# Kernel optimization log

Measured on AMD Instinct MI355X. Metric: run time of the kernel, lower is better.

## Reference

```python
import jax, jax.numpy as jnp
import numpy as np

DIM = 256
HEADS = 8
B, T, D, H, W = 2, 8, 16, 16, 16


def _mha(x, wqkv, bqkv, wo, bo):
    # x: [M, S, F]; standard self-attention (q=k=v=x), LoRA rank 0.
    M, S, F = x.shape
    hd = F // HEADS
    qkv = jnp.einsum('msf,kfg->kmsg', x, wqkv) + bqkv[:, None, None, :]  # [3,M,S,F]
    q, k, v = qkv
    q = q.reshape(M, S, HEADS, hd).transpose(0, 2, 1, 3)  # [M,Hh,S,hd]
    k = k.reshape(M, S, HEADS, hd).transpose(0, 2, 1, 3)
    v = v.reshape(M, S, HEADS, hd).transpose(0, 2, 1, 3)
    scores = jnp.einsum('mhsd,mhtd->mhst', q, k) / jnp.sqrt(jnp.asarray(hd, x.dtype))
    attn = jax.nn.softmax(scores, axis=-1)
    out = jnp.einsum('mhst,mhtd->mhsd', attn, v)
    out = out.transpose(0, 2, 1, 3).reshape(M, S, F)
    return out @ wo + bo


def _make_params(key, name_suffix):
    k1, k2 = jax.random.split(key)
    s = 1.0 / np.sqrt(DIM)
    return {
        f'wqkv_{name_suffix}': jax.random.normal(k1, (3, DIM, DIM), jnp.float32) * s,
        f'bqkv_{name_suffix}': jnp.zeros((3, DIM), jnp.float32),
        f'wo_{name_suffix}': jax.random.normal(k2, (DIM, DIM), jnp.float32) * s,
        f'bo_{name_suffix}': jnp.zeros((DIM,), jnp.float32),
    }


def setup_inputs() -> dict:
    key = jax.random.key(0)
    ks = jax.random.split(key, 5)
    inp = {'x': jax.random.normal(ks[0], (B, T, D * H * W, DIM), jnp.float32)}
    for k, ax in zip(ks[1:], ['t', 'd', 'h', 'w']):
        inp.update(_make_params(k, ax))
    inp['grid_d'] = D
    inp['grid_h'] = H
    inp['grid_w'] = W
    return inp


def reference(x, wqkv_t, bqkv_t, wo_t, bo_t,
              wqkv_d, bqkv_d, wo_d, bo_d,
              wqkv_h, bqkv_h, wo_h, bo_h,
              wqkv_w, bqkv_w, wo_w, bo_w,
              grid_d, grid_h, grid_w):
    b, t, n, f = x.shape
    d, h, w = grid_d, grid_h, grid_w
    x = x.reshape(b, t, d, h, w, f)
    if t > 1:
        xt = x.transpose(0, 2, 3, 4, 1, 5).reshape(b * d * h * w, t, f)
        xt = _mha(xt, wqkv_t, bqkv_t, wo_t, bo_t)
        xt = xt.reshape(b, d, h, w, t, f).transpose(0, 4, 1, 2, 3, 5)
        x = x + xt
    xd = x.transpose(0, 1, 3, 4, 2, 5).reshape(b * t * h * w, d, f)
    xd = _mha(xd, wqkv_d, bqkv_d, wo_d, bo_d)
    xd = xd.reshape(b, t, h, w, d, f).transpose(0, 1, 4, 2, 3, 5)
    xh = x.transpose(0, 1, 2, 4, 3, 5).reshape(b * t * d * w, h, f)
    xh = _mha(xh, wqkv_h, bqkv_h, wo_h, bo_h)
    xh = xh.reshape(b, t, d, w, h, f).transpose(0, 1, 2, 4, 3, 5)
    xw = x.reshape(b * t * d * h, w, f)
    xw = _mha(xw, wqkv_w, bqkv_w, wo_w, bo_w)
    xw = xw.reshape(b, t, d, h, w, f)
    x_comb = x + xd + xh + xw
    return x_comb.reshape(b, t, d * h * w, f)
```

## Files before the change

kernel.cpp:

```cpp
#include <hip/hip_runtime.h>

typedef __attribute__((ext_vector_type(4))) float f32x4;
typedef __attribute__((ext_vector_type(8))) short s16x8;

__device__ __forceinline__ ushort f2bf(float f) {
  union { float f; uint u; } v; v.f = f;
  uint r = v.u + 0x7fffu + ((v.u >> 16) & 1u);
  return (ushort)(r >> 16);
}

__device__ __forceinline__ void glds16(const void* g, void* l) {
  __builtin_amdgcn_global_load_lds(
      (const __attribute__((address_space(1))) uint*)g,
      (__attribute__((address_space(3))) uint*)l, 16, 0, 0);
}

__device__ __forceinline__ int asidx(int row, int col) {
  return row*256 + ((((col>>3) ^ (row & 7)))<<3) + (col&7);
}
__device__ __forceinline__ int scridx(int row, int col) {
  return row*32 + ((((col>>3) ^ ((row>>2)&3)))<<3) + (col&7);
}
__device__ __forceinline__ int epidx(int row, int f) {
  return row*256 + (f ^ ((row & 7) << 2));
}

struct WSrc { const float* p[8]; };

__global__ __launch_bounds__(256) void prep_weights(WSrc s, ushort* wq, ushort* wo) {
  int mm = blockIdx.x >> 6;
  int t  = blockIdx.x & 63;
  int a = mm >> 2, sub = mm & 3;
  const float* src = (sub < 3) ? (s.p[a*2] + sub*65536) : s.p[a*2+1];
  ushort*      dst = (sub < 3) ? (wq + (a*3 + sub)*65536) : (wo + a*65536);
  int gt = (t >> 3) * 32, ft = (t & 7) * 32;
  __shared__ float tile[32][33];
  int lx = threadIdx.x & 31, ly = threadIdx.x >> 5;
#pragma unroll
  for (int i = 0; i < 4; i++)
    tile[ly + i*8][lx] = src[(ft + ly + i*8)*256 + gt + lx];
  __syncthreads();
#pragma unroll
  for (int i = 0; i < 4; i++) {
    int n = gt + ly + i*8, col = ft + lx;
    dst[asidx(n, col)] = f2bf(tile[lx][ly + i*8]);
  }
}

template<int AXIS>
__device__ __forceinline__ int token_index(int blk, int row) {
  if (AXIS == 0) {
    int seq = blk*8 + (row >> 3);
    int t = row & 7;
    int b = seq >> 12, n = seq & 4095;
    return (b*8 + t)*4096 + n;
  } else {
    int sid = blk*4 + (row >> 4);
    int bt = sid >> 8, lo = sid & 255, r = row & 15;
    if (AXIS == 1) { int hh = lo >> 4, ww = lo & 15; return bt*4096 + r*256 + hh*16 + ww; }
    if (AXIS == 2) { int dd = lo >> 4, ww = lo & 15; return bt*4096 + dd*256 + r*16 + ww; }
    { int dd = lo >> 4, hh = lo & 15; return bt*4096 + dd*256 + hh*16 + r; }
  }
}

#define PUB_BARRIER() do { \
    __builtin_amdgcn_sched_barrier(0); \
    asm volatile("s_waitcnt lgkmcnt(0)" ::: "memory"); \
    __builtin_amdgcn_sched_barrier(0); \
    __builtin_amdgcn_s_barrier(); \
    __builtin_amdgcn_sched_barrier(0); } while (0)

template<int AXIS>
__global__ __launch_bounds__(256, 2) void axial_pass(
    const float* __restrict__ x0, const ushort* __restrict__ xb,
    const ushort* __restrict__ wqkvT, const float* __restrict__ bqkv,
    const ushort* __restrict__ woT, const float* __restrict__ bo,
    float* __restrict__ out, ushort* __restrict__ x1b) {

  __shared__ ushort smem[40960];
  ushort* Wb0 = smem;
  ushort* Wb1 = smem + 8192;
  ushort* AsT = smem + 16384;
  ushort* Scr = smem + 32768;

  const int tid = threadIdx.x, blk = blockIdx.x;
  const int wv = tid >> 6, lane = tid & 63, llo = lane & 15, lhi = lane >> 4;
  const int rg = wv >> 1, ch = wv & 1;
  const f32x4 fzero = {0.f, 0.f, 0.f, 0.f};
  const s16x8 szero = {0,0,0,0,0,0,0,0};

  auto issue_stage = [&](int s) {
    const ushort* src = (s < 24) ? (wqkvT + (s % 3)*65536 + (s / 3)*8192)
                                 : (woT + (s - 24)*8192);
    const ushort* g = src + wv*2048 + lane*8;
    ushort* l = ((s & 1) ? Wb1 : Wb0) + wv*2048;
#pragma unroll
    for (int i = 0; i < 4; i++) glds16(g + i*512, l + i*512);
  };

#define STAGE_SYNC(sn) do { \
    __builtin_amdgcn_sched_barrier(0); \
    asm volatile("s_waitcnt vmcnt(0) lgkmcnt(0)" ::: "memory"); \
    __builtin_amdgcn_sched_barrier(0); \
    __builtin_amdgcn_s_barrier(); \
    __builtin_amdgcn_sched_barrier(0); \
    if ((sn) < 32) issue_stage(sn); \
  } while (0)

  issue_stage(0);

  {
    int row = tid >> 2, q = tid & 3;
    int tok = token_index<AXIS>(blk, row);
    if (AXIS == 0) {
      const float4* s4 = (const float4*)(x0 + (size_t)tok*256 + q*64);
#pragma unroll
      for (int c2 = 0; c2 < 8; c2++) {
        float4 v0 = s4[c2*2], v1 = s4[c2*2 + 1];
        s16x8 o;
        o[0] = (short)f2bf(v0.x); o[1] = (short)f2bf(v0.y);
        o[2] = (short)f2bf(v0.z); o[3] = (short)f2bf(v0.w);
        o[4] = (short)f2bf(v1.x); o[5] = (short)f2bf(v1.y);
        o[6] = (short)f2bf(v1.z); o[7] = (short)f2bf(v1.w);
        *(s16x8*)(AsT + asidx(row, (q*8 + c2)*8)) = o;
      }
    } else {
      const s16x8* s8 = (const s16x8*)(xb + (size_t)tok*256 + q*64);
#pragma unroll
      for (int c2 = 0; c2 < 8; c2++)
        *(s16x8*)(AsT + asidx(row, (q*8 + c2)*8)) = s8[c2];
    }
  }
  {
    ushort* Vtw = Scr + wv*2048 + 1024;
    *(s16x8*)(Vtw + scridx(lane >> 1, 16 + (lane & 1)*8)) = szero;
  }
  __syncthreads();

  s16x8 af[2][8];
#pragma unroll
  for (int g = 0; g < 2; g++)
#pragma unroll
    for (int ks = 0; ks < 8; ks++)
      af[g][ks] = *(const s16x8*)(AsT + asidx(rg*32 + g*16 + llo, (ks*4 + lhi)*8));

  auto proj2 = [&](int sb, f32x4& c0, f32x4& c1) {
    const ushort* buf = sb ? Wb1 : Wb0;
    __builtin_amdgcn_s_setprio(1);
#pragma unroll
    for (int ks = 0; ks < 8; ks++) {
      s16x8 bv = *(const s16x8*)(buf + asidx(ch*16 + llo, (ks*4 + lhi)*8));
      c0 = __builtin_amdgcn_mfma_f32_16x16x32_bf16(af[0][ks], bv, c0, 0, 0, 0);
      c1 = __builtin_amdgcn_mfma_f32_16x16x32_bf16(af[1][ks], bv, c1, 0, 0, 0);
    }
    __builtin_amdgcn_s_setprio(0);
  };

#pragma unroll 1
  for (int h = 0; h < 8; h++) {
    STAGE_SYNC(3*h + 1);
    {
      f32x4 c0 = fzero, c1 = fzero;
      proj2((3*h) & 1, c0, c1);
      float bi = bqkv[h*32 + ch*16 + llo];
      ushort* q0 = Scr + (rg*2 + 0)*2048;
      ushort* q1 = Scr + (rg*2 + 1)*2048;
#pragma unroll
      for (int r = 0; r < 4; r++) {
        q0[scridx(lhi*4 + r, ch*16 + llo)] = f2bf(c0[r] + bi);
        q1[scridx(lhi*4 + r, ch*16 + llo)] = f2bf(c1[r] + bi);
      }
    }
    STAGE_SYNC(3*h + 2);
    {
      f32x4 c0 = fzero, c1 = fzero;
      proj2((3*h + 1) & 1, c0, c1);
      float bi = bqkv[256 + h*32 + ch*16 + llo];
      ushort* k0 = Scr + (rg*2 + 0)*2048 + 512;
      ushort* k1 = Scr + (rg*2 + 1)*2048 + 512;
#pragma unroll
      for (int r = 0; r < 4; r++) {
        k0[scridx(lhi*4 + r, ch*16 + llo)] = f2bf(c0[r] + bi);
        k1[scridx(lhi*4 + r, ch*16 + llo)] = f2bf(c1[r] + bi);
      }
    }
    STAGE_SYNC(3*h + 3);
    {
      f32x4 c0 = fzero, c1 = fzero;
      proj2((3*h + 2) & 1, c0, c1);
      float bi = bqkv[512 + h*32 + ch*16 + llo];
      ushort* v0 = Scr + (rg*2 + 0)*2048 + 1024;
      ushort* v1 = Scr + (rg*2 + 1)*2048 + 1024;
#pragma unroll
      for (int r = 0; r < 4; r++) {
        v0[scridx(ch*16 + llo, lhi*4 + r)] = f2bf(c0[r] + bi);
        v1[scridx(ch*16 + llo, lhi*4 + r)] = f2bf(c1[r] + bi);
      }
    }
    PUB_BARRIER();

    {
      ushort* S = Scr + wv*2048;
      s16x8 aq = *(const s16x8*)(S + scridx(llo, lhi*8));
      s16x8 bk = *(const s16x8*)(S + 512 + scridx(llo, lhi*8));
      f32x4 sc = __builtin_amdgcn_mfma_f32_16x16x32_bf16(aq, bk, fzero, 0, 0, 0);
#pragma unroll
      for (int r = 0; r < 4; r++) {
        float sv = sc[r] * 0.17677669529663689f;
        if (AXIS == 0) {
          int srow = lhi*4 + r;
          if ((srow >> 3) != (llo >> 3)) sv = -1e30f;
        }
        float mx = sv;
        mx = fmaxf(mx, __shfl_xor(mx, 1));
        mx = fmaxf(mx, __shfl_xor(mx, 2));
        mx = fmaxf(mx, __shfl_xor(mx, 4));
        mx = fmaxf(mx, __shfl_xor(mx, 8));
        float e = __expf(sv - mx);
        float sm = e;
        sm += __shfl_xor(sm, 1);
        sm += __shfl_xor(sm, 2);
        sm += __shfl_xor(sm, 4);
        sm += __shfl_xor(sm, 8);
        (S + 512)[scridx(lhi*4 + r, llo)] = f2bf(e * __builtin_amdgcn_rcpf(sm));
      }
      s16x8 ap  = *(const s16x8*)(S + 512 + scridx(llo, lhi*8));
      s16x8 bv0 = *(const s16x8*)(S + 1024 + scridx(llo, lhi*8));
      s16x8 bv1 = *(const s16x8*)(S + 1024 + scridx(16 + llo, lhi*8));
      f32x4 o0 = __builtin_amdgcn_mfma_f32_16x16x32_bf16(ap, bv0, fzero, 0, 0, 0);
      f32x4 o1 = __builtin_amdgcn_mfma_f32_16x16x32_bf16(ap, bv1, fzero, 0, 0, 0);
#pragma unroll
      for (int r = 0; r < 4; r++) {
        AsT[asidx(wv*16 + lhi*4 + r, h*32 + llo)]      = f2bf(o0[r]);
        AsT[asidx(wv*16 + lhi*4 + r, h*32 + 16 + llo)] = f2bf(o1[r]);
      }
    }
  }

  PUB_BARRIER();

#pragma unroll
  for (int g = 0; g < 2; g++)
#pragma unroll
    for (int ks = 0; ks < 8; ks++)
      af[g][ks] = *(const s16x8*)(AsT + asidx(rg*32 + g*16 + llo, (ks*4 + lhi)*8));

  f32x4 acc[16];
#pragma unroll
  for (int i = 0; i < 16; i++) acc[i] = fzero;
#pragma unroll
  for (int st = 0; st < 8; st++) {
    STAGE_SYNC(25 + st);
    const ushort* buf = (st & 1) ? Wb1 : Wb0;
    __builtin_amdgcn_s_setprio(1);
#pragma unroll
    for (int ks = 0; ks < 8; ks++) {
      s16x8 bv = *(const s16x8*)(buf + asidx(ch*16 + llo, (ks*4 + lhi)*8));
      acc[st*2]   = __builtin_amdgcn_mfma_f32_16x16x32_bf16(af[0][ks], bv, acc[st*2],   0, 0, 0);
      acc[st*2+1] = __builtin_amdgcn_mfma_f32_16x16x32_bf16(af[1][ks], bv, acc[st*2+1], 0, 0, 0);
    }
    __builtin_amdgcn_s_setprio(0);
  }

  float* Fep = (float*)smem;
  PUB_BARRIER();
#pragma unroll
  for (int st = 0; st < 8; st++) {
#pragma unroll
    for (int g = 0; g < 2; g++) {
#pragma unroll
      for (int r = 0; r < 4; r++) {
        int row = rg*32 + g*16 + lhi*4 + r;
        Fep[epidx(row, st*32 + ch*16 + llo)] = acc[st*2 + g][r];
      }
    }
  }
  PUB_BARRIER();
  {
    int rbase = tid >> 3, g = tid & 7;
#pragma unroll 1
    for (int step = 0; step < 2; step++) {
      int row = rbase + step*32;
      int tok = token_index<AXIS>(blk, row);
      size_t base = (size_t)tok*256;
#pragma unroll
      for (int i = 0; i < 8; i++) {
        int f = i*32 + g*4;
        float4 v = *(float4*)&Fep[epidx(row, f)];
        float4 b = *(const float4*)&bo[f];
        v.x += b.x; v.y += b.y; v.z += b.z; v.w += b.w;
        if (AXIS == 0) {
          float4 x = *(const float4*)&x0[base + f];
          v.x += x.x; v.y += x.y; v.z += x.z; v.w += x.w;
          *(float4*)&out[base + f] = v;
          ushort4 p; p.x = f2bf(v.x); p.y = f2bf(v.y);
          p.z = f2bf(v.z); p.w = f2bf(v.w);
          *(ushort4*)&x1b[base + f] = p;
        } else {
          float4 o = *(float4*)&out[base + f];
          o.x += v.x; o.y += v.y; o.z += v.z; o.w += v.w;
          *(float4*)&out[base + f] = o;
        }
      }
    }
  }
#undef STAGE_SYNC
}

extern "C" void kernel_launch(void* const* d_in, const int* in_sizes, int n_in,
                              void* d_out, int out_size, void* d_ws, size_t ws_size,
                              hipStream_t stream) {
  const float* x = (const float*)d_in[0];
  ushort* wq  = (ushort*)d_ws;
  ushort* wo  = wq + 4*3*65536;
  ushort* x1b = wo + 4*65536;
  float* out = (float*)d_out;

  WSrc wsrc;
  wsrc.p[0] = (const float*)d_in[1];  wsrc.p[1] = (const float*)d_in[3];
  wsrc.p[2] = (const float*)d_in[5];  wsrc.p[3] = (const float*)d_in[7];
  wsrc.p[4] = (const float*)d_in[9];  wsrc.p[5] = (const float*)d_in[11];
  wsrc.p[6] = (const float*)d_in[13]; wsrc.p[7] = (const float*)d_in[15];
  prep_weights<<<dim3(1024), dim3(256), 0, stream>>>(wsrc, wq, wo);

  const float* bq_t = (const float*)d_in[2];  const float* bo_t = (const float*)d_in[4];
  const float* bq_d = (const float*)d_in[6];  const float* bo_d = (const float*)d_in[8];
  const float* bq_h = (const float*)d_in[10]; const float* bo_h = (const float*)d_in[12];
  const float* bq_w = (const float*)d_in[14]; const float* bo_w = (const float*)d_in[16];

  axial_pass<0><<<dim3(1024), dim3(256), 0, stream>>>(x, nullptr, wq + 0*3*65536, bq_t, wo + 0*65536, bo_t, out, x1b);
  axial_pass<1><<<dim3(1024), dim3(256), 0, stream>>>(nullptr, x1b, wq + 1*3*65536, bq_d, wo + 1*65536, bo_d, out, nullptr);
  axial_pass<2><<<dim3(1024), dim3(256), 0, stream>>>(nullptr, x1b, wq + 2*3*65536, bq_h, wo + 2*65536, bo_h, out, nullptr);
  axial_pass<3><<<dim3(1024), dim3(256), 0, stream>>>(nullptr, x1b, wq + 3*3*65536, bq_w, wo + 3*65536, bo_w, out, nullptr);
}
```

Baseline: 351.0 us.

## Double block size to 512 threads and keep attention output in registers

Each block now handles 128 token rows with 8 waves, so every streamed weight stage in LDS is reused by twice as many rows and only half as many blocks are launched. The separate activation buffer in LDS is dropped: input rows are staged through the scratch area in two halves, and each wave keeps its attention output fragments in registers for the output projection instead of writing them back to shared memory. The epilogue goes through LDS in bf16 rather than fp32, with wider 8-element accesses. The trade-off is higher register pressure from the extra fragments and the fully unrolled head loop, plus extra rounding of the projection result before the bias and residual add.

Result: slower. 415.7 us (+18.4%).

```diff
diff --git a/kernel.cpp b/kernel.cpp
--- a/kernel.cpp
+++ b/kernel.cpp
@@ -8,6 +8,9 @@
   uint r = v.u + 0x7fffu + ((v.u >> 16) & 1u);
   return (ushort)(r >> 16);
 }
+__device__ __forceinline__ float bf2f(ushort u) {
+  union { uint i; float f; } v; v.i = ((uint)u) << 16; return v.f;
+}
 
 __device__ __forceinline__ void glds16(const void* g, void* l) {
   __builtin_amdgcn_global_load_lds(
@@ -20,9 +23,6 @@
 }
 __device__ __forceinline__ int scridx(int row, int col) {
   return row*32 + ((((col>>3) ^ ((row>>2)&3)))<<3) + (col&7);
-}
-__device__ __forceinline__ int epidx(int row, int f) {
-  return row*256 + (f ^ ((row & 7) << 2));
 }
 
 struct WSrc { const float* p[8]; };
@@ -50,12 +50,12 @@
 template<int AXIS>
 __device__ __forceinline__ int token_index(int blk, int row) {
   if (AXIS == 0) {
-    int seq = blk*8 + (row >> 3);
+    int seq = blk*16 + (row >> 3);
     int t = row & 7;
     int b = seq >> 12, n = seq & 4095;
     return (b*8 + t)*4096 + n;
   } else {
-    int sid = blk*4 + (row >> 4);
+    int sid = blk*8 + (row >> 4);
     int bt = sid >> 8, lo = sid & 255, r = row & 15;
     if (AXIS == 1) { int hh = lo >> 4, ww = lo & 15; return bt*4096 + r*256 + hh*16 + ww; }
     if (AXIS == 2) { int dd = lo >> 4, ww = lo & 15; return bt*4096 + dd*256 + r*16 + ww; }
@@ -71,17 +71,16 @@
     __builtin_amdgcn_sched_barrier(0); } while (0)
 
 template<int AXIS>
-__global__ __launch_bounds__(256, 2) void axial_pass(
+__global__ __launch_bounds__(512, 4) void axial_pass(
     const float* __restrict__ x0, const ushort* __restrict__ xb,
     const ushort* __restrict__ wqkvT, const float* __restrict__ bqkv,
     const ushort* __restrict__ woT, const float* __restrict__ bo,
     float* __restrict__ out, ushort* __restrict__ x1b) {
 
-  __shared__ ushort smem[40960];
+  __shared__ ushort smem[32768];
   ushort* Wb0 = smem;
   ushort* Wb1 = smem + 8192;
-  ushort* AsT = smem + 16384;
-  ushort* Scr = smem + 32768;
+  ushort* Scr = smem + 16384;
 
   const int tid = threadIdx.x, blk = blockIdx.x;
   const int wv = tid >> 6, lane = tid & 63, llo = lane & 15, lhi = lane >> 4;
@@ -92,10 +91,10 @@
   auto issue_stage = [&](int s) {
     const ushort* src = (s < 24) ? (wqkvT + (s % 3)*65536 + (s / 3)*8192)
                                  : (woT + (s - 24)*8192);
-    const ushort* g = src + wv*2048 + lane*8;
-    ushort* l = ((s & 1) ? Wb1 : Wb0) + wv*2048;
-#pragma unroll
-    for (int i = 0; i < 4; i++) glds16(g + i*512, l + i*512);
+    const ushort* g = src + wv*1024 + lane*8;
+    ushort* l = ((s & 1) ? Wb1 : Wb0) + wv*1024;
+    glds16(g, l);
+    glds16(g + 512, l + 512);
   };
 
 #define STAGE_SYNC(sn) do { \
@@ -109,40 +108,57 @@
 
   issue_stage(0);
 
-  {
-    int row = tid >> 2, q = tid & 3;
-    int tok = token_index<AXIS>(blk, row);
+  s16x8 af[2][8];
+  auto stage_half = [&](int half) {
+    int row = tid >> 3, j = tid & 7;
+    int tok = token_index<AXIS>(blk, half*64 + row);
     if (AXIS == 0) {
-      const float4* s4 = (const float4*)(x0 + (size_t)tok*256 + q*64);
-#pragma unroll
-      for (int c2 = 0; c2 < 8; c2++) {
-        float4 v0 = s4[c2*2], v1 = s4[c2*2 + 1];
+      const float4* s4 = (const float4*)(x0 + (size_t)tok*256);
+#pragma unroll
+      for (int i = 0; i < 4; i++) {
+        int c = j + 8*i;
+        float4 v0 = s4[c*2], v1 = s4[c*2 + 1];
         s16x8 o;
         o[0] = (short)f2bf(v0.x); o[1] = (short)f2bf(v0.y);
         o[2] = (short)f2bf(v0.z); o[3] = (short)f2bf(v0.w);
         o[4] = (short)f2bf(v1.x); o[5] = (short)f2bf(v1.y);
         o[6] = (short)f2bf(v1.z); o[7] = (short)f2bf(v1.w);
-        *(s16x8*)(AsT + asidx(row, (q*8 + c2)*8)) = o;
+        *(s16x8*)(Scr + asidx(row, c*8)) = o;
       }
     } else {
-      const s16x8* s8 = (const s16x8*)(xb + (size_t)tok*256 + q*64);
-#pragma unroll
-      for (int c2 = 0; c2 < 8; c2++)
-        *(s16x8*)(AsT + asidx(row, (q*8 + c2)*8)) = s8[c2];
-    }
-  }
+      const s16x8* s8 = (const s16x8*)(xb + (size_t)tok*256);
+#pragma unroll
+      for (int i = 0; i < 4; i++) {
+        int c = j + 8*i;
+        *(s16x8*)(Scr + asidx(row, c*8)) = s8[c];
+      }
+    }
+  };
+
+  stage_half(0);
+  __syncthreads();
+  if (wv < 4) {
+#pragma unroll
+    for (int g = 0; g < 2; g++)
+#pragma unroll
+      for (int ks = 0; ks < 8; ks++)
+        af[g][ks] = *(const s16x8*)(Scr + asidx(rg*32 + g*16 + llo, (ks*4 + lhi)*8));
+  }
+  __syncthreads();
+  stage_half(1);
+  __syncthreads();
+  if (wv >= 4) {
+#pragma unroll
+    for (int g = 0; g < 2; g++)
+#pragma unroll
+      for (int ks = 0; ks < 8; ks++)
+        af[g][ks] = *(const s16x8*)(Scr + asidx((rg - 2)*32 + g*16 + llo, (ks*4 + lhi)*8));
+  }
+  __syncthreads();
   {
     ushort* Vtw = Scr + wv*2048 + 1024;
     *(s16x8*)(Vtw + scridx(lane >> 1, 16 + (lane & 1)*8)) = szero;
   }
-  __syncthreads();
-
-  s16x8 af[2][8];
-#pragma unroll
-  for (int g = 0; g < 2; g++)
-#pragma unroll
-    for (int ks = 0; ks < 8; ks++)
-      af[g][ks] = *(const s16x8*)(AsT + asidx(rg*32 + g*16 + llo, (ks*4 + lhi)*8));
 
   auto proj2 = [&](int sb, f32x4& c0, f32x4& c1) {
     const ushort* buf = sb ? Wb1 : Wb0;
@@ -156,7 +172,9 @@
     __builtin_amdgcn_s_setprio(0);
   };
 
-#pragma unroll 1
+  s16x8 af_o[8];
+
+#pragma unroll
   for (int h = 0; h < 8; h++) {
     STAGE_SYNC(3*h + 1);
     {
@@ -231,19 +249,12 @@
       f32x4 o1 = __builtin_amdgcn_mfma_f32_16x16x32_bf16(ap, bv1, fzero, 0, 0, 0);
 #pragma unroll
       for (int r = 0; r < 4; r++) {
-        AsT[asidx(wv*16 + lhi*4 + r, h*32 + llo)]      = f2bf(o0[r]);
-        AsT[asidx(wv*16 + lhi*4 + r, h*32 + 16 + llo)] = f2bf(o1[r]);
-      }
-    }
-  }
-
-  PUB_BARRIER();
-
-#pragma unroll
-  for (int g = 0; g < 2; g++)
-#pragma unroll
-    for (int ks = 0; ks < 8; ks++)
-      af[g][ks] = *(const s16x8*)(AsT + asidx(rg*32 + g*16 + llo, (ks*4 + lhi)*8));
+        S[scridx(lhi*4 + r, llo)]      = f2bf(o0[r]);
+        S[scridx(lhi*4 + r, 16 + llo)] = f2bf(o1[r]);
+      }
+      af_o[h] = *(const s16x8*)(S + scridx(llo, lhi*8));
+    }
+  }
 
   f32x4 acc[16];
 #pragma unroll
@@ -255,52 +266,59 @@
     __builtin_amdgcn_s_setprio(1);
 #pragma unroll
     for (int ks = 0; ks < 8; ks++) {
-      s16x8 bv = *(const s16x8*)(buf + asidx(ch*16 + llo, (ks*4 + lhi)*8));
-      acc[st*2]   = __builtin_amdgcn_mfma_f32_16x16x32_bf16(af[0][ks], bv, acc[st*2],   0, 0, 0);
-      acc[st*2+1] = __builtin_amdgcn_mfma_f32_16x16x32_bf16(af[1][ks], bv, acc[st*2+1], 0, 0, 0);
+      s16x8 b0 = *(const s16x8*)(buf + asidx(llo,      (ks*4 + lhi)*8));
+      s16x8 b1 = *(const s16x8*)(buf + asidx(16 + llo, (ks*4 + lhi)*8));
+      acc[st*2]   = __builtin_amdgcn_mfma_f32_16x16x32_bf16(af_o[ks], b0, acc[st*2],   0, 0, 0);
+      acc[st*2+1] = __builtin_amdgcn_mfma_f32_16x16x32_bf16(af_o[ks], b1, acc[st*2+1], 0, 0, 0);
     }
     __builtin_amdgcn_s_setprio(0);
   }
 
-  float* Fep = (float*)smem;
+  ushort* Fep = smem;
   PUB_BARRIER();
 #pragma unroll
   for (int st = 0; st < 8; st++) {
 #pragma unroll
-    for (int g = 0; g < 2; g++) {
-#pragma unroll
-      for (int r = 0; r < 4; r++) {
-        int row = rg*32 + g*16 + lhi*4 + r;
-        Fep[epidx(row, st*32 + ch*16 + llo)] = acc[st*2 + g][r];
+    for (int j = 0; j < 2; j++) {
+#pragma unroll
+      for (int r = 0; r < 4; r++) {
+        int row = wv*16 + lhi*4 + r;
+        Fep[asidx(row, st*32 + j*16 + llo)] = f2bf(acc[st*2 + j][r]);
       }
     }
   }
   PUB_BARRIER();
   {
-    int rbase = tid >> 3, g = tid & 7;
-#pragma unroll 1
-    for (int step = 0; step < 2; step++) {
-      int row = rbase + step*32;
-      int tok = token_index<AXIS>(blk, row);
-      size_t base = (size_t)tok*256;
-#pragma unroll
-      for (int i = 0; i < 8; i++) {
-        int f = i*32 + g*4;
-        float4 v = *(float4*)&Fep[epidx(row, f)];
-        float4 b = *(const float4*)&bo[f];
-        v.x += b.x; v.y += b.y; v.z += b.z; v.w += b.w;
-        if (AXIS == 0) {
-          float4 x = *(const float4*)&x0[base + f];
-          v.x += x.x; v.y += x.y; v.z += x.z; v.w += x.w;
-          *(float4*)&out[base + f] = v;
-          ushort4 p; p.x = f2bf(v.x); p.y = f2bf(v.y);
-          p.z = f2bf(v.z); p.w = f2bf(v.w);
-          *(ushort4*)&x1b[base + f] = p;
-        } else {
-          float4 o = *(float4*)&out[base + f];
-          o.x += v.x; o.y += v.y; o.z += v.z; o.w += v.w;
-          *(float4*)&out[base + f] = o;
-        }
+    int row = tid >> 2, q = tid & 3;
+    int tok = token_index<AXIS>(blk, row);
+    size_t base = (size_t)tok*256;
+#pragma unroll
+    for (int i = 0; i < 8; i++) {
+      int col = q*64 + i*8;
+      s16x8 v8 = *(const s16x8*)(Fep + asidx(row, col));
+      float f[8];
+#pragma unroll
+      for (int j = 0; j < 8; j++) f[j] = bf2f((ushort)v8[j]) + bo[col + j];
+      if (AXIS == 0) {
+        float4 xa = *(const float4*)&x0[base + col];
+        float4 xb4 = *(const float4*)&x0[base + col + 4];
+        float4 va = {f[0]+xa.x, f[1]+xa.y, f[2]+xa.z, f[3]+xa.w};
+        float4 vb = {f[4]+xb4.x, f[5]+xb4.y, f[6]+xb4.z, f[7]+xb4.w};
+        *(float4*)&out[base + col]     = va;
+        *(float4*)&out[base + col + 4] = vb;
+        s16x8 p;
+        p[0] = (short)f2bf(va.x); p[1] = (short)f2bf(va.y);
+        p[2] = (short)f2bf(va.z); p[3] = (short)f2bf(va.w);
+        p[4] = (short)f2bf(vb.x); p[5] = (short)f2bf(vb.y);
+        p[6] = (short)f2bf(vb.z); p[7] = (short)f2bf(vb.w);
+        *(s16x8*)&x1b[base + col] = p;
+      } else {
+        float4 oa = *(float4*)&out[base + col];
+        float4 ob = *(float4*)&out[base + col + 4];
+        oa.x += f[0]; oa.y += f[1]; oa.z += f[2]; oa.w += f[3];
+        ob.x += f[4]; ob.y += f[5]; ob.z += f[6]; ob.w += f[7];
+        *(float4*)&out[base + col]     = oa;
+        *(float4*)&out[base + col + 4] = ob;
       }
     }
   }
@@ -328,8 +346,8 @@
   const float* bq_h = (const float*)d_in[10]; const float* bo_h = (const float*)d_in[12];
   const float* bq_w = (const float*)d_in[14]; const float* bo_w = (const float*)d_in[16];
 
-  axial_pass<0><<<dim3(1024), dim3(256), 0, stream>>>(x, nullptr, wq + 0*3*65536, bq_t, wo + 0*65536, bo_t, out, x1b);
-  axial_pass<1><<<dim3(1024), dim3(256), 0, stream>>>(nullptr, x1b, wq + 1*3*65536, bq_d, wo + 1*65536, bo_d, out, nullptr);
-  axial_pass<2><<<dim3(1024), dim3(256), 0, stream>>>(nullptr, x1b, wq + 2*3*65536, bq_h, wo + 2*65536, bo_h, out, nullptr);
-  axial_pass<3><<<dim3(1024), dim3(256), 0, stream>>>(nullptr, x1b, wq + 3*3*65536, bq_w, wo + 3*65536, bo_w, out, nullptr);
-}
+  axial_pass<0><<<dim3(512), dim3(512), 0, stream>>>(x, nullptr, wq + 0*3*65536, bq_t, wo + 0*65536, bo_t, out, x1b);
+  axial_pass<1><<<dim3(512), dim3(512), 0, stream>>>(nullptr, x1b, wq + 1*3*65536, bq_d, wo + 1*65536, bo_d, out, nullptr);
+  axial_pass<2><<<dim3(512), dim3(512), 0, stream>>>(nullptr, x1b, wq + 2*3*65536, bq_h, wo + 2*65536, bo_h, out, nullptr);
+  axial_pass<3><<<dim3(512), dim3(512), 0, stream>>>(nullptr, x1b, wq + 3*3*65536, bq_w, wo + 3*65536, bo_w, out, nullptr);
+}
```

## Fuse output projection into per-head loop and shrink LDS for higher occupancy

Applied to the files above, without the earlier changes.

The output projection now runs per head inside the attention loop. Each head's attention output (16 rows x 32 dims per wave) is multiplied against a head-sliced Wo tile that prep_weights reorders into a new layout, and the results accumulate in registers. This removes the full-width attention-output staging buffer in LDS, cutting shared memory from 80KB to 48KB so launch bounds can allow 3 blocks per CU. In exchange the epilogue now rounds the fp32 projection accumulators to bf16 in LDS before adding the bias and residual, which loses precision. The kernel also issues one extra stage sync per head.

Result: slower. 462.9 us (+31.9%).

```diff
diff --git a/kernel.cpp b/kernel.cpp
--- a/kernel.cpp
+++ b/kernel.cpp
@@ -8,6 +8,9 @@
   uint r = v.u + 0x7fffu + ((v.u >> 16) & 1u);
   return (ushort)(r >> 16);
 }
+__device__ __forceinline__ float bf2f(ushort u) {
+  union { uint i; float f; } v; v.i = ((uint)u) << 16; return v.f;
+}
 
 __device__ __forceinline__ void glds16(const void* g, void* l) {
   __builtin_amdgcn_global_load_lds(
@@ -20,9 +23,6 @@
 }
 __device__ __forceinline__ int scridx(int row, int col) {
   return row*32 + ((((col>>3) ^ ((row>>2)&3)))<<3) + (col&7);
-}
-__device__ __forceinline__ int epidx(int row, int f) {
-  return row*256 + (f ^ ((row & 7) << 2));
 }
 
 struct WSrc { const float* p[8]; };
@@ -42,8 +42,10 @@
   __syncthreads();
 #pragma unroll
   for (int i = 0; i < 4; i++) {
-    int n = gt + ly + i*8, col = ft + lx;
-    dst[asidx(n, col)] = f2bf(tile[lx][ly + i*8]);
+    int n = gt + ly + i*8, k = ft + lx;
+    float v = tile[lx][ly + i*8];
+    if (sub < 3) dst[asidx(n, k)] = f2bf(v);
+    else         dst[(k >> 5)*8192 + (n >> 4)*512 + scridx(n & 15, k & 31)] = f2bf(v);
   }
 }
 
@@ -71,17 +73,16 @@
     __builtin_amdgcn_sched_barrier(0); } while (0)
 
 template<int AXIS>
-__global__ __launch_bounds__(256, 2) void axial_pass(
+__global__ __launch_bounds__(256, 3) void axial_pass(
     const float* __restrict__ x0, const ushort* __restrict__ xb,
     const ushort* __restrict__ wqkvT, const float* __restrict__ bqkv,
-    const ushort* __restrict__ woT, const float* __restrict__ bo,
+    const ushort* __restrict__ woR, const float* __restrict__ bo,
     float* __restrict__ out, ushort* __restrict__ x1b) {
 
-  __shared__ ushort smem[40960];
+  __shared__ ushort smem[24576];
   ushort* Wb0 = smem;
   ushort* Wb1 = smem + 8192;
-  ushort* AsT = smem + 16384;
-  ushort* Scr = smem + 32768;
+  ushort* Scr = smem + 16384;
 
   const int tid = threadIdx.x, blk = blockIdx.x;
   const int wv = tid >> 6, lane = tid & 63, llo = lane & 15, lhi = lane >> 4;
@@ -90,8 +91,9 @@
   const s16x8 szero = {0,0,0,0,0,0,0,0};
 
   auto issue_stage = [&](int s) {
-    const ushort* src = (s < 24) ? (wqkvT + (s % 3)*65536 + (s / 3)*8192)
-                                 : (woT + (s - 24)*8192);
+    int h = s >> 2, m = s & 3;
+    const ushort* src = (m < 3) ? (wqkvT + m*65536 + h*8192)
+                                 : (woR + h*8192);
     const ushort* g = src + wv*2048 + lane*8;
     ushort* l = ((s & 1) ? Wb1 : Wb0) + wv*2048;
 #pragma unroll
@@ -106,8 +108,6 @@
     __builtin_amdgcn_sched_barrier(0); \
     if ((sn) < 32) issue_stage(sn); \
   } while (0)
-
-  issue_stage(0);
 
   {
     int row = tid >> 2, q = tid & 3;
@@ -122,13 +122,13 @@
         o[2] = (short)f2bf(v0.z); o[3] = (short)f2bf(v0.w);
         o[4] = (short)f2bf(v1.x); o[5] = (short)f2bf(v1.y);
         o[6] = (short)f2bf(v1.z); o[7] = (short)f2bf(v1.w);
-        *(s16x8*)(AsT + asidx(row, (q*8 + c2)*8)) = o;
+        *(s16x8*)(smem + asidx(row, (q*8 + c2)*8)) = o;
       }
     } else {
       const s16x8* s8 = (const s16x8*)(xb + (size_t)tok*256 + q*64);
 #pragma unroll
       for (int c2 = 0; c2 < 8; c2++)
-        *(s16x8*)(AsT + asidx(row, (q*8 + c2)*8)) = s8[c2];
+        *(s16x8*)(smem + asidx(row, (q*8 + c2)*8)) = s8[c2];
     }
   }
   {
@@ -142,7 +142,10 @@
   for (int g = 0; g < 2; g++)
 #pragma unroll
     for (int ks = 0; ks < 8; ks++)
-      af[g][ks] = *(const s16x8*)(AsT + asidx(rg*32 + g*16 + llo, (ks*4 + lhi)*8));
+      af[g][ks] = *(const s16x8*)(smem + asidx(rg*32 + g*16 + llo, (ks*4 + lhi)*8));
+  __syncthreads();
+
+  issue_stage(0);
 
   auto proj2 = [&](int sb, f32x4& c0, f32x4& c1) {
     const ushort* buf = sb ? Wb1 : Wb0;
@@ -156,12 +159,16 @@
     __builtin_amdgcn_s_setprio(0);
   };
 
+  f32x4 acc[16];
+#pragma unroll
+  for (int i = 0; i < 16; i++) acc[i] = fzero;
+
 #pragma unroll 1
   for (int h = 0; h < 8; h++) {
-    STAGE_SYNC(3*h + 1);
+    STAGE_SYNC(4*h + 1);
     {
       f32x4 c0 = fzero, c1 = fzero;
-      proj2((3*h) & 1, c0, c1);
+      proj2((4*h) & 1, c0, c1);
       float bi = bqkv[h*32 + ch*16 + llo];
       ushort* q0 = Scr + (rg*2 + 0)*2048;
       ushort* q1 = Scr + (rg*2 + 1)*2048;
@@ -171,10 +178,10 @@
         q1[scridx(lhi*4 + r, ch*16 + llo)] = f2bf(c1[r] + bi);
       }
     }
-    STAGE_SYNC(3*h + 2);
+    STAGE_SYNC(4*h + 2);
     {
       f32x4 c0 = fzero, c1 = fzero;
-      proj2((3*h + 1) & 1, c0, c1);
+      proj2((4*h + 1) & 1, c0, c1);
       float bi = bqkv[256 + h*32 + ch*16 + llo];
       ushort* k0 = Scr + (rg*2 + 0)*2048 + 512;
       ushort* k1 = Scr + (rg*2 + 1)*2048 + 512;
@@ -184,10 +191,11 @@
         k1[scridx(lhi*4 + r, ch*16 + llo)] = f2bf(c1[r] + bi);
       }
     }
-    STAGE_SYNC(3*h + 3);
+    STAGE_SYNC(4*h + 3);
+    s16x8 af_o;
     {
       f32x4 c0 = fzero, c1 = fzero;
-      proj2((3*h + 2) & 1, c0, c1);
+      proj2((4*h + 2) & 1, c0, c1);
       float bi = bqkv[512 + h*32 + ch*16 + llo];
       ushort* v0 = Scr + (rg*2 + 0)*2048 + 1024;
       ushort* v1 = Scr + (rg*2 + 1)*2048 + 1024;
@@ -196,10 +204,8 @@
         v0[scridx(ch*16 + llo, lhi*4 + r)] = f2bf(c0[r] + bi);
         v1[scridx(ch*16 + llo, lhi*4 + r)] = f2bf(c1[r] + bi);
       }
-    }
-    PUB_BARRIER();
-
-    {
+      PUB_BARRIER();
+
       ushort* S = Scr + wv*2048;
       s16x8 aq = *(const s16x8*)(S + scridx(llo, lhi*8));
       s16x8 bk = *(const s16x8*)(S + 512 + scridx(llo, lhi*8));
@@ -231,49 +237,32 @@
       f32x4 o1 = __builtin_amdgcn_mfma_f32_16x16x32_bf16(ap, bv1, fzero, 0, 0, 0);
 #pragma unroll
       for (int r = 0; r < 4; r++) {
-        AsT[asidx(wv*16 + lhi*4 + r, h*32 + llo)]      = f2bf(o0[r]);
-        AsT[asidx(wv*16 + lhi*4 + r, h*32 + 16 + llo)] = f2bf(o1[r]);
-      }
-    }
-  }
-
+        S[scridx(lhi*4 + r, llo)]      = f2bf(o0[r]);
+        S[scridx(lhi*4 + r, 16 + llo)] = f2bf(o1[r]);
+      }
+      af_o = *(const s16x8*)(S + scridx(llo, lhi*8));
+    }
+    STAGE_SYNC(4*h + 4);
+    {
+      const ushort* buf = ((4*h + 3) & 1) ? Wb1 : Wb0;
+      const int so = scridx(llo, lhi*8);
+      __builtin_amdgcn_s_setprio(1);
+#pragma unroll
+      for (int nb = 0; nb < 16; nb++) {
+        s16x8 bw = *(const s16x8*)(buf + nb*512 + so);
+        acc[nb] = __builtin_amdgcn_mfma_f32_16x16x32_bf16(af_o, bw, acc[nb], 0, 0, 0);
+      }
+      __builtin_amdgcn_s_setprio(0);
+    }
+  }
+
+  ushort* Fep = smem;
   PUB_BARRIER();
-
-#pragma unroll
-  for (int g = 0; g < 2; g++)
-#pragma unroll
-    for (int ks = 0; ks < 8; ks++)
-      af[g][ks] = *(const s16x8*)(AsT + asidx(rg*32 + g*16 + llo, (ks*4 + lhi)*8));
-
-  f32x4 acc[16];
-#pragma unroll
-  for (int i = 0; i < 16; i++) acc[i] = fzero;
-#pragma unroll
-  for (int st = 0; st < 8; st++) {
-    STAGE_SYNC(25 + st);
-    const ushort* buf = (st & 1) ? Wb1 : Wb0;
-    __builtin_amdgcn_s_setprio(1);
-#pragma unroll
-    for (int ks = 0; ks < 8; ks++) {
-      s16x8 bv = *(const s16x8*)(buf + asidx(ch*16 + llo, (ks*4 + lhi)*8));
-      acc[st*2]   = __builtin_amdgcn_mfma_f32_16x16x32_bf16(af[0][ks], bv, acc[st*2],   0, 0, 0);
-      acc[st*2+1] = __builtin_amdgcn_mfma_f32_16x16x32_bf16(af[1][ks], bv, acc[st*2+1], 0, 0, 0);
-    }
-    __builtin_amdgcn_s_setprio(0);
-  }
-
-  float* Fep = (float*)smem;
-  PUB_BARRIER();
-#pragma unroll
-  for (int st = 0; st < 8; st++) {
-#pragma unroll
-    for (int g = 0; g < 2; g++) {
-#pragma unroll
-      for (int r = 0; r < 4; r++) {
-        int row = rg*32 + g*16 + lhi*4 + r;
-        Fep[epidx(row, st*32 + ch*16 + llo)] = acc[st*2 + g][r];
-      }
-    }
+#pragma unroll
+  for (int nb = 0; nb < 16; nb++) {
+#pragma unroll
+    for (int r = 0; r < 4; r++)
+      Fep[asidx(wv*16 + lhi*4 + r, nb*16 + llo)] = f2bf(acc[nb][r]);
   }
   PUB_BARRIER();
   {
@@ -285,21 +274,22 @@
       size_t base = (size_t)tok*256;
 #pragma unroll
       for (int i = 0; i < 8; i++) {
-        int f = i*32 + g*4;
-        float4 v = *(float4*)&Fep[epidx(row, f)];
-        float4 b = *(const float4*)&bo[f];
-        v.x += b.x; v.y += b.y; v.z += b.z; v.w += b.w;
+        int col = i*32 + g*4;
+        const ushort* fp = Fep + asidx(row, col);
+        float4 b = *(const float4*)&bo[col];
+        float4 v = {bf2f(fp[0]) + b.x, bf2f(fp[1]) + b.y,
+                    bf2f(fp[2]) + b.z, bf2f(fp[3]) + b.w};
         if (AXIS == 0) {
-          float4 x = *(const float4*)&x0[base + f];
+          float4 x = *(const float4*)&x0[base + col];
           v.x += x.x; v.y += x.y; v.z += x.z; v.w += x.w;
-          *(float4*)&out[base + f] = v;
+          *(float4*)&out[base + col] = v;
           ushort4 p; p.x = f2bf(v.x); p.y = f2bf(v.y);
           p.z = f2bf(v.z); p.w = f2bf(v.w);
-          *(ushort4*)&x1b[base + f] = p;
+          *(ushort4*)&x1b[base + col] = p;
         } else {
-          float4 o = *(float4*)&out[base + f];
+          float4 o = *(float4*)&out[base + col];
           o.x += v.x; o.y += v.y; o.z += v.z; o.w += v.w;
-          *(float4*)&out[base + f] = o;
+          *(float4*)&out[base + col] = o;
         }
       }
     }
```

## Use per-wave private weight buffers with vmcnt pipelining to drop block barriers

Applied to the files above, without the earlier changes.

The QKV projection weight staging changes from a block-shared double buffer guarded by a full barrier per stage to per-wave private copies of each wave's column half. These are prefetched two stages ahead and waited on with a partial vmcnt, so most block-wide barriers in the projection loop disappear. Each wave's attention output is now kept in registers and written back to a shared A tile only once, after the head loop. The cost is twice the weight bytes loaded into LDS, since both row-group waves fetch the same slice, plus a full unroll of the head loop that raises register pressure.

Measured after the change: 392.4 us. 1.12x slower.

```diff
diff --git a/kernel.cpp b/kernel.cpp
--- a/kernel.cpp
+++ b/kernel.cpp
@@ -78,9 +78,6 @@
     float* __restrict__ out, ushort* __restrict__ x1b) {
 
   __shared__ ushort smem[40960];
-  ushort* Wb0 = smem;
-  ushort* Wb1 = smem + 8192;
-  ushort* AsT = smem + 16384;
   ushort* Scr = smem + 32768;
 
   const int tid = threadIdx.x, blk = blockIdx.x;
@@ -89,25 +86,24 @@
   const f32x4 fzero = {0.f, 0.f, 0.f, 0.f};
   const s16x8 szero = {0,0,0,0,0,0,0,0};
 
-  auto issue_stage = [&](int s) {
-    const ushort* src = (s < 24) ? (wqkvT + (s % 3)*65536 + (s / 3)*8192)
-                                 : (woT + (s - 24)*8192);
-    const ushort* g = src + wv*2048 + lane*8;
-    ushort* l = ((s & 1) ? Wb1 : Wb0) + wv*2048;
-#pragma unroll
-    for (int i = 0; i < 4; i++) glds16(g + i*512, l + i*512);
+  auto issue_priv = [&](int s) {
+    const ushort* g = wqkvT + (s % 3)*65536 + (s / 3)*8192 + ch*4096 + lane*8;
+    ushort* l = smem + (s & 1)*16384 + wv*4096 + lane*8;
+#pragma unroll
+    for (int i = 0; i < 8; i++) glds16(g + i*512, l + i*512);
   };
 
-#define STAGE_SYNC(sn) do { \
-    __builtin_amdgcn_sched_barrier(0); \
-    asm volatile("s_waitcnt vmcnt(0) lgkmcnt(0)" ::: "memory"); \
-    __builtin_amdgcn_sched_barrier(0); \
-    __builtin_amdgcn_s_barrier(); \
-    __builtin_amdgcn_sched_barrier(0); \
-    if ((sn) < 32) issue_stage(sn); \
+#define WAIT_STAGE(s) do { \
+    if ((s) <= 22) { asm volatile("s_waitcnt vmcnt(8)" ::: "memory"); } \
+    else           { asm volatile("s_waitcnt vmcnt(0)" ::: "memory"); } \
+    __builtin_amdgcn_sched_barrier(0); \
   } while (0)
-
-  issue_stage(0);
+#define ISSUE_NEXT(s) do { \
+    __builtin_amdgcn_sched_barrier(0); \
+    asm volatile("s_waitcnt lgkmcnt(0)" ::: "memory"); \
+    __builtin_amdgcn_sched_barrier(0); \
+    if ((s) + 2 <= 23) issue_priv((s) + 2); \
+  } while (0)
 
   {
     int row = tid >> 2, q = tid & 3;
@@ -122,13 +118,13 @@
         o[2] = (short)f2bf(v0.z); o[3] = (short)f2bf(v0.w);
         o[4] = (short)f2bf(v1.x); o[5] = (short)f2bf(v1.y);
         o[6] = (short)f2bf(v1.z); o[7] = (short)f2bf(v1.w);
-        *(s16x8*)(AsT + asidx(row, (q*8 + c2)*8)) = o;
+        *(s16x8*)(smem + asidx(row, (q*8 + c2)*8)) = o;
       }
     } else {
       const s16x8* s8 = (const s16x8*)(xb + (size_t)tok*256 + q*64);
 #pragma unroll
       for (int c2 = 0; c2 < 8; c2++)
-        *(s16x8*)(AsT + asidx(row, (q*8 + c2)*8)) = s8[c2];
+        *(s16x8*)(smem + asidx(row, (q*8 + c2)*8)) = s8[c2];
     }
   }
   {
@@ -142,26 +138,30 @@
   for (int g = 0; g < 2; g++)
 #pragma unroll
     for (int ks = 0; ks < 8; ks++)
-      af[g][ks] = *(const s16x8*)(AsT + asidx(rg*32 + g*16 + llo, (ks*4 + lhi)*8));
-
-  auto proj2 = [&](int sb, f32x4& c0, f32x4& c1) {
-    const ushort* buf = sb ? Wb1 : Wb0;
-    __builtin_amdgcn_s_setprio(1);
-#pragma unroll
-    for (int ks = 0; ks < 8; ks++) {
-      s16x8 bv = *(const s16x8*)(buf + asidx(ch*16 + llo, (ks*4 + lhi)*8));
-      c0 = __builtin_amdgcn_mfma_f32_16x16x32_bf16(af[0][ks], bv, c0, 0, 0, 0);
-      c1 = __builtin_amdgcn_mfma_f32_16x16x32_bf16(af[1][ks], bv, c1, 0, 0, 0);
-    }
-    __builtin_amdgcn_s_setprio(0);
-  };
-
-#pragma unroll 1
+      af[g][ks] = *(const s16x8*)(smem + asidx(rg*32 + g*16 + llo, (ks*4 + lhi)*8));
+  __syncthreads();
+
+  issue_priv(0);
+  issue_priv(1);
+
+  s16x8 af_o[8];
+
+#pragma unroll
   for (int h = 0; h < 8; h++) {
-    STAGE_SYNC(3*h + 1);
     {
+      const int s = 3*h;
+      WAIT_STAGE(s);
+      const ushort* wbuf = smem + (s & 1)*16384 + wv*4096;
       f32x4 c0 = fzero, c1 = fzero;
-      proj2((3*h) & 1, c0, c1);
+      __builtin_amdgcn_s_setprio(1);
+#pragma unroll
+      for (int ks = 0; ks < 8; ks++) {
+        s16x8 bv = *(const s16x8*)(wbuf + asidx(llo, (ks*4 + lhi)*8));
+        c0 = __builtin_amdgcn_mfma_f32_16x16x32_bf16(af[0][ks], bv, c0, 0, 0, 0);
+        c1 = __builtin_amdgcn_mfma_f32_16x16x32_bf16(af[1][ks], bv, c1, 0, 0, 0);
+      }
+      __builtin_amdgcn_s_setprio(0);
+      ISSUE_NEXT(s);
       float bi = bqkv[h*32 + ch*16 + llo];
       ushort* q0 = Scr + (rg*2 + 0)*2048;
       ushort* q1 = Scr + (rg*2 + 1)*2048;
@@ -171,10 +171,20 @@
         q1[scridx(lhi*4 + r, ch*16 + llo)] = f2bf(c1[r] + bi);
       }
     }
-    STAGE_SYNC(3*h + 2);
     {
+      const int s = 3*h + 1;
+      WAIT_STAGE(s);
+      const ushort* wbuf = smem + (s & 1)*16384 + wv*4096;
       f32x4 c0 = fzero, c1 = fzero;
-      proj2((3*h + 1) & 1, c0, c1);
+      __builtin_amdgcn_s_setprio(1);
+#pragma unroll
+      for (int ks = 0; ks < 8; ks++) {
+        s16x8 bv = *(const s16x8*)(wbuf + asidx(llo, (ks*4 + lhi)*8));
+        c0 = __builtin_amdgcn_mfma_f32_16x16x32_bf16(af[0][ks], bv, c0, 0, 0, 0);
+        c1 = __builtin_amdgcn_mfma_f32_16x16x32_bf16(af[1][ks], bv, c1, 0, 0, 0);
+      }
+      __builtin_amdgcn_s_setprio(0);
+      ISSUE_NEXT(s);
       float bi = bqkv[256 + h*32 + ch*16 + llo];
       ushort* k0 = Scr + (rg*2 + 0)*2048 + 512;
       ushort* k1 = Scr + (rg*2 + 1)*2048 + 512;
@@ -184,10 +194,20 @@
         k1[scridx(lhi*4 + r, ch*16 + llo)] = f2bf(c1[r] + bi);
       }
     }
-    STAGE_SYNC(3*h + 3);
     {
+      const int s = 3*h + 2;
+      WAIT_STAGE(s);
+      const ushort* wbuf = smem + (s & 1)*16384 + wv*4096;
       f32x4 c0 = fzero, c1 = fzero;
-      proj2((3*h + 2) & 1, c0, c1);
+      __builtin_amdgcn_s_setprio(1);
+#pragma unroll
+      for (int ks = 0; ks < 8; ks++) {
+        s16x8 bv = *(const s16x8*)(wbuf + asidx(llo, (ks*4 + lhi)*8));
+        c0 = __builtin_amdgcn_mfma_f32_16x16x32_bf16(af[0][ks], bv, c0, 0, 0, 0);
+        c1 = __builtin_amdgcn_mfma_f32_16x16x32_bf16(af[1][ks], bv, c1, 0, 0, 0);
+      }
+      __builtin_amdgcn_s_setprio(0);
+      ISSUE_NEXT(s);
       float bi = bqkv[512 + h*32 + ch*16 + llo];
       ushort* v0 = Scr + (rg*2 + 0)*2048 + 1024;
       ushort* v1 = Scr + (rg*2 + 1)*2048 + 1024;
@@ -196,10 +216,8 @@
         v0[scridx(ch*16 + llo, lhi*4 + r)] = f2bf(c0[r] + bi);
         v1[scridx(ch*16 + llo, lhi*4 + r)] = f2bf(c1[r] + bi);
       }
-    }
-    PUB_BARRIER();
-
-    {
+      PUB_BARRIER();
+
       ushort* S = Scr + wv*2048;
       s16x8 aq = *(const s16x8*)(S + scridx(llo, lhi*8));
       s16x8 bk = *(const s16x8*)(S + 512 + scridx(llo, lhi*8));
@@ -231,13 +249,27 @@
       f32x4 o1 = __builtin_amdgcn_mfma_f32_16x16x32_bf16(ap, bv1, fzero, 0, 0, 0);
 #pragma unroll
       for (int r = 0; r < 4; r++) {
-        AsT[asidx(wv*16 + lhi*4 + r, h*32 + llo)]      = f2bf(o0[r]);
-        AsT[asidx(wv*16 + lhi*4 + r, h*32 + 16 + llo)] = f2bf(o1[r]);
-      }
-    }
-  }
-
+        S[scridx(lhi*4 + r, llo)]      = f2bf(o0[r]);
+        S[scridx(lhi*4 + r, 16 + llo)] = f2bf(o1[r]);
+      }
+      af_o[h] = *(const s16x8*)(S + scridx(llo, lhi*8));
+      PUB_BARRIER();
+    }
+  }
+
+  ushort* AsT = smem + 16384;
+#pragma unroll
+  for (int ks = 0; ks < 8; ks++)
+    *(s16x8*)(AsT + asidx(wv*16 + llo, (ks*4 + lhi)*8)) = af_o[ks];
   PUB_BARRIER();
+
+  auto issue_shared = [&](int st) {
+    const ushort* g = woT + st*8192 + wv*2048 + lane*8;
+    ushort* l = smem + (st & 1)*8192 + wv*2048;
+#pragma unroll
+    for (int i = 0; i < 4; i++) glds16(g + i*512, l + i*512);
+  };
+  issue_shared(0);
 
 #pragma unroll
   for (int g = 0; g < 2; g++)
@@ -250,8 +282,13 @@
   for (int i = 0; i < 16; i++) acc[i] = fzero;
 #pragma unroll
   for (int st = 0; st < 8; st++) {
-    STAGE_SYNC(25 + st);
-    const ushort* buf = (st & 1) ? Wb1 : Wb0;
+    __builtin_amdgcn_sched_barrier(0);
+    asm volatile("s_waitcnt vmcnt(0) lgkmcnt(0)" ::: "memory");
+    __builtin_amdgcn_sched_barrier(0);
+    __builtin_amdgcn_s_barrier();
+    __builtin_amdgcn_sched_barrier(0);
+    if (st + 1 < 8) issue_shared(st + 1);
+    const ushort* buf = smem + (st & 1)*8192;
     __builtin_amdgcn_s_setprio(1);
 #pragma unroll
     for (int ks = 0; ks < 8; ks++) {
@@ -304,7 +341,8 @@
       }
     }
   }
-#undef STAGE_SYNC
+#undef WAIT_STAGE
+#undef ISSUE_NEXT
 }
 
 extern "C" void kernel_launch(void* const* d_in, const int* in_sizes, int n_in,
```
